# Optimization experiments

Hardware: AMD Instinct MI355X
Metric: run time of the kernel (lower is better)

The kernel has to match this reference:

```python
import jax, jax.numpy as jnp
import numpy as np

NBITS = 8          # attn_nbits
GROUP = 32         # per-group size along head_dim for Q/K quantizers
H = 16             # num_heads
EPS = 1e-8


def _ste(x, q):
    # straight-through estimator: forward=q, backward=identity
    return x + jax.lax.stop_gradient(q - x)


def pg_dynamic_quant(x, group_size=GROUP, nbits=NBITS):
    """Per-group symmetric dynamic fake-quant along last dim (ActPGDynamicQuantizer)."""
    qmax = 2.0 ** (nbits - 1) - 1
    lead, D = x.shape[:-1], x.shape[-1]
    xg = x.reshape(*lead, D // group_size, group_size)
    s = jnp.maximum(jnp.max(jnp.abs(xg), axis=-1, keepdims=True) / qmax, EPS)
    q = jnp.clip(jnp.round(xg / s), -qmax - 1.0, qmax) * s
    return _ste(x, q.reshape(x.shape))


def dynamic_quant(x, axis=2, nbits=NBITS):
    """Symmetric dynamic fake-quant, scale shared along `axis` (ActDynamicQuantizer)."""
    qmax = 2.0 ** (nbits - 1) - 1
    s = jnp.maximum(jnp.max(jnp.abs(x), axis=axis, keepdims=True) / qmax, EPS)
    q = jnp.clip(jnp.round(x / s), -qmax - 1.0, qmax) * s
    return _ste(x, q)


def static_scale_quant(x, nbits=NBITS):
    """Unsigned static-scale fake-quant for softmax map in [0,1] (ActStaticScaleQuantizer)."""
    qmax = 2.0 ** nbits - 1
    q = jnp.clip(jnp.round(x * qmax), 0.0, qmax) / qmax
    return _ste(x, q)


def setup_inputs() -> dict:
    key = jax.random.key(0)
    ks = jax.random.split(key, 7)
    B, L, C = 4, 1024, 1024
    return {
        "x":         jax.random.normal(ks[0], (B, L, C), jnp.float32),
        "attn_bias": jax.random.normal(ks[1], (1, 1, L, L), jnp.float32) * 0.1,
        "w_qkv":     jax.random.normal(ks[2], (3 * C, C), jnp.float32) * 0.02,
        "q_bias":    jax.random.normal(ks[3], (C,), jnp.float32) * 0.02,
        "v_bias":    jax.random.normal(ks[4], (C,), jnp.float32) * 0.02,
        "w_proj":    jax.random.normal(ks[5], (C, C), jnp.float32) * 0.02,
        "b_proj":    jax.random.normal(ks[6], (C,), jnp.float32) * 0.02,
    }


def reference(x, attn_bias, w_qkv, q_bias, v_bias, w_proj, b_proj):
    B, L, C = x.shape
    D = C // H
    scale = D ** -0.5
    # qkv projection: bias-free linear + concat(q_bias, zeros_k, v_bias)
    bias = jnp.concatenate([q_bias, jnp.zeros_like(q_bias), v_bias])
    qkv = (x @ w_qkv.T + bias).reshape(B, L, 3, H, D)
    q, k, v = jnp.transpose(qkv, (2, 0, 3, 1, 4))  # each [B,H,L,D]
    # inline fake-quantization (MODE 0 inference path)
    qq = pg_dynamic_quant(q)
    kk = pg_dynamic_quant(k)
    vv = dynamic_quant(v, axis=2)
    attn = jnp.einsum('bhld,bhmd->bhlm', qq * scale, kk) + attn_bias  # [B,H,L,L]
    a = jax.nn.softmax(attn, axis=-1)
    a = static_scale_quant(a)
    out = jnp.einsum('bhlm,bhmd->bhld', a, vv)
    out = jnp.transpose(out, (0, 2, 1, 3)).reshape(B, L, C)
    return out @ w_proj.T + b_proj
```

## Files before the change

### kernel.cpp

```cpp
#include <hip/hip_runtime.h>


typedef unsigned short u16;
typedef unsigned int u32;
typedef __attribute__((ext_vector_type(8))) _Float16 half8;
typedef __attribute__((ext_vector_type(4))) float f32x4;

__device__ __forceinline__ u16 f2b(float f) {
    u32 i;
    __builtin_memcpy(&i, &f, 4);
    return (u16)((i + 0x7FFFu + ((i >> 16) & 1u)) >> 16);
}

__device__ __forceinline__ void split16(float v, u16& hi, u16& lo) {
    _Float16 h = (_Float16)v;
    _Float16 l = (_Float16)(v - (float)h);
    __builtin_memcpy(&hi, &h, 2);
    __builtin_memcpy(&lo, &l, 2);
}

__device__ __forceinline__ int dot4(int a, int b, int c) {
#if __has_builtin(__builtin_amdgcn_sdot4)
    return __builtin_amdgcn_sdot4(a, b, c, false);
#else
    int r = c;
    r += ((a << 24) >> 24) * ((b << 24) >> 24);
    r += ((a << 16) >> 24) * ((b << 16) >> 24);
    r += ((a << 8) >> 24) * ((b << 8) >> 24);
    r += (a >> 24) * (b >> 24);
    return r;
#endif
}

__device__ __forceinline__ double fexp(double x) {
    double kd = rint(x * 1.4426950408889634);
    double r = fma(kd, -6.93147180369123816490e-01, x);
    r = fma(kd, -1.90821492927058770002e-10, r);
    double p = 2.7557319223985888e-07;
    p = fma(p, r, 2.7557319223985890e-06);
    p = fma(p, r, 2.4801587301587302e-05);
    p = fma(p, r, 1.9841269841269841e-04);
    p = fma(p, r, 1.3888888888888889e-03);
    p = fma(p, r, 8.3333333333333333e-03);
    p = fma(p, r, 4.1666666666666664e-02);
    p = fma(p, r, 1.6666666666666666e-01);
    p = fma(p, r, 0.5);
    p = fma(p, r, 1.0);
    p = fma(p, r, 1.0);
    long long bits;
    __builtin_memcpy(&bits, &p, 8);
    bits += ((long long)kd) << 52;
    double e;
    __builtin_memcpy(&e, &bits, 8);
    return (x < -700.0) ? 0.0 : e;
}

__global__ __launch_bounds__(256) void cvt_bf16w(u16* __restrict__ dst,
                                                 const float* __restrict__ src, int n) {
    int i = (blockIdx.x * 256 + threadIdx.x) * 4;
    if (i + 3 < n) {
        float4 v = *(const float4*)(src + i);
        ushort4 o;
        o.x = f2b(v.x); o.y = f2b(v.y); o.z = f2b(v.z); o.w = f2b(v.w);
        *(ushort4*)(dst + i) = o;
    }
}

__global__ __launch_bounds__(256) void gemm_qkv3(const float* __restrict__ A,
                                                 const float* __restrict__ Bm,
                                                 const float* __restrict__ qbias,
                                                 const float* __restrict__ vbias,
                                                 float* __restrict__ qws,
                                                 float* __restrict__ kws,
                                                 float* __restrict__ vws) {
    __shared__ u16 Ah[128 * 32], Al[128 * 32], Bh[64 * 32], Bl[64 * 32];
    const int t = threadIdx.x;
    const int lane = t & 63, w = t >> 6;
    const int srow = t >> 2, scol = (t & 3) * 8;
    const int lm = lane & 15, lk = (lane >> 4) * 8;
    const int bm = blockIdx.y, bn = blockIdx.x;

    const float* ap = A + (size_t)(bm * 128 + srow) * 1024 + scol;
    const float* bp = Bm + (size_t)(bn * 64 + srow) * 1024 + scol;

    double dacc[2][4][4];
#pragma unroll
    for (int i = 0; i < 2; i++)
#pragma unroll
        for (int j = 0; j < 4; j++)
#pragma unroll
            for (int r = 0; r < 4; r++) dacc[i][j][r] = 0.0;

    for (int slab = 0; slab < 8; slab++) {
        f32x4 acc[2][4];
#pragma unroll
        for (int i = 0; i < 2; i++)
#pragma unroll
            for (int j = 0; j < 4; j++) acc[i][j] = (f32x4){0.f, 0.f, 0.f, 0.f};

        for (int kc = 0; kc < 4; kc++) {
            const int k0 = slab * 128 + kc * 32;
            float vreg[3][8];
#pragma unroll
            for (int e = 0; e < 3; e++) {
                const float* src = (e < 2) ? (ap + e * (size_t)64 * 1024 + k0)
                                           : (bp + k0);
                float4 v0 = *(const float4*)(src);
                float4 v1 = *(const float4*)(src + 4);
                vreg[e][0] = v0.x; vreg[e][1] = v0.y; vreg[e][2] = v0.z; vreg[e][3] = v0.w;
                vreg[e][4] = v1.x; vreg[e][5] = v1.y; vreg[e][6] = v1.z; vreg[e][7] = v1.w;
            }
            __syncthreads();
#pragma unroll
            for (int e = 0; e < 3; e++) {
                union { u16 us[8]; uint4 v; } ph, pl;
#pragma unroll
                for (int j = 0; j < 8; j++) split16(vreg[e][j], ph.us[j], pl.us[j]);
                u16* dh = (e < 2) ? Ah : Bh;
                u16* dl = (e < 2) ? Al : Bl;
                int row = (e < 2) ? (srow + e * 64) : srow;
                *(uint4*)(dh + row * 32 + scol) = ph.v;
                *(uint4*)(dl + row * 32 + scol) = pl.v;
            }
            __syncthreads();

            half8 fah[2], fal[2], fbh[4], fbl[4];
#pragma unroll
            for (int i = 0; i < 2; i++) {
                int ra = (w * 32 + i * 16 + lm) * 32 + lk;
                fah[i] = *(const half8*)(Ah + ra);
                fal[i] = *(const half8*)(Al + ra);
            }
#pragma unroll
            for (int i = 0; i < 4; i++) {
                int rb = (i * 16 + lm) * 32 + lk;
                fbh[i] = *(const half8*)(Bh + rb);
                fbl[i] = *(const half8*)(Bl + rb);
            }
#pragma unroll
            for (int mi = 0; mi < 2; mi++)
#pragma unroll
                for (int ni = 0; ni < 4; ni++) {
                    acc[mi][ni] = __builtin_amdgcn_mfma_f32_16x16x32_f16(
                        fal[mi], fbh[ni], acc[mi][ni], 0, 0, 0);
                    acc[mi][ni] = __builtin_amdgcn_mfma_f32_16x16x32_f16(
                        fah[mi], fbl[ni], acc[mi][ni], 0, 0, 0);
                    acc[mi][ni] = __builtin_amdgcn_mfma_f32_16x16x32_f16(
                        fah[mi], fbh[ni], acc[mi][ni], 0, 0, 0);
                }
        }
#pragma unroll
        for (int i = 0; i < 2; i++)
#pragma unroll
            for (int j = 0; j < 4; j++)
#pragma unroll
                for (int r = 0; r < 4; r++) dacc[i][j][r] += (double)acc[i][j][r];
    }

    const int rbase = bm * 128 + w * 32 + (lane >> 4) * 4;
    const int cbase = bn * 64 + lm;
#pragma unroll
    for (int mi = 0; mi < 2; mi++)
#pragma unroll
        for (int ni = 0; ni < 4; ni++) {
            int col = cbase + ni * 16;
            int sel = col >> 10, cc = col & 1023;
            double bias = (sel == 0) ? (double)qbias[cc]
                        : ((sel == 2) ? (double)vbias[cc] : 0.0);
            float* dst = (sel == 0) ? qws : ((sel == 1) ? kws : vws);
#pragma unroll
            for (int r = 0; r < 4; r++) {
                int row = rbase + mi * 16 + r;
                dst[(size_t)row * 1024 + cc] = (float)(dacc[mi][ni][r] + bias);
            }
        }
}

__global__ __launch_bounds__(256) void quant_qk(const float* __restrict__ pre,
                                                signed char* __restrict__ qout,
                                                double* __restrict__ sout) {
    size_t g = (size_t)blockIdx.x * 256 + threadIdx.x;
    const float* p = pre + g * 32;
    float v[32];
    float amax = 0.f;
#pragma unroll
    for (int i = 0; i < 8; i++) {
        float4 q4 = ((const float4*)p)[i];
        v[i * 4 + 0] = q4.x; v[i * 4 + 1] = q4.y; v[i * 4 + 2] = q4.z; v[i * 4 + 3] = q4.w;
        amax = fmaxf(amax, fmaxf(fmaxf(fabsf(q4.x), fabsf(q4.y)),
                                 fmaxf(fabsf(q4.z), fabsf(q4.w))));
    }
    double s = fmax((double)amax / 127.0, 1e-8);
    sout[g] = s;
    int pk[8];
#pragma unroll
    for (int i = 0; i < 8; i++) {
        int b0 = (int)fmin(fmax(rint((double)v[i * 4 + 0] / s), -128.0), 127.0);
        int b1 = (int)fmin(fmax(rint((double)v[i * 4 + 1] / s), -128.0), 127.0);
        int b2 = (int)fmin(fmax(rint((double)v[i * 4 + 2] / s), -128.0), 127.0);
        int b3 = (int)fmin(fmax(rint((double)v[i * 4 + 3] / s), -128.0), 127.0);
        pk[i] = (b0 & 255) | ((b1 & 255) << 8) | ((b2 & 255) << 16) | ((b3 & 255) << 24);
    }
    int4* d = (int4*)(qout + g * 32);
    d[0] = make_int4(pk[0], pk[1], pk[2], pk[3]);
    d[1] = make_int4(pk[4], pk[5], pk[6], pk[7]);
}

__global__ __launch_bounds__(256) void quant_k(const float* __restrict__ pre,
                                               int* __restrict__ kT,
                                               double* __restrict__ ksT) {
    size_t g = (size_t)blockIdx.x * 256 + threadIdx.x;
    const float* p = pre + g * 32;
    float v[32];
    float amax = 0.f;
#pragma unroll
    for (int i = 0; i < 8; i++) {
        float4 q4 = ((const float4*)p)[i];
        v[i * 4 + 0] = q4.x; v[i * 4 + 1] = q4.y; v[i * 4 + 2] = q4.z; v[i * 4 + 3] = q4.w;
        amax = fmaxf(amax, fmaxf(fmaxf(fabsf(q4.x), fabsf(q4.y)),
                                 fmaxf(fabsf(q4.z), fabsf(q4.w))));
    }
    double s = fmax((double)amax / 127.0, 1e-8);
    int pk[8];
#pragma unroll
    for (int i = 0; i < 8; i++) {
        int b0 = (int)fmin(fmax(rint((double)v[i * 4 + 0] / s), -128.0), 127.0);
        int b1 = (int)fmin(fmax(rint((double)v[i * 4 + 1] / s), -128.0), 127.0);
        int b2 = (int)fmin(fmax(rint((double)v[i * 4 + 2] / s), -128.0), 127.0);
        int b3 = (int)fmin(fmax(rint((double)v[i * 4 + 3] / s), -128.0), 127.0);
        pk[i] = (b0 & 255) | ((b1 & 255) << 8) | ((b2 & 255) << 16) | ((b3 & 255) << 24);
    }
    const int m = (int)((g >> 5) & 1023);
    const int b = (int)(g >> 15);
    const int sub = (int)(g & 31);
    const int h = sub >> 1, pp = sub & 1;
    const int bh = b * 16 + h;
    int* dst = kT + ((size_t)bh * 16 + pp * 8) * 1024 + m;
#pragma unroll
    for (int i = 0; i < 8; i++) dst[i * 1024] = pk[i];
    ksT[((size_t)bh * 2 + pp) * 1024 + m] = s;
}

__global__ __launch_bounds__(256) void vmax_part(const float* __restrict__ vws,
                                                 float* __restrict__ pmax) {
    const int lc = blockIdx.x, b = blockIdx.y, t = threadIdx.x;
#pragma unroll
    for (int j = 0; j < 4; j++) {
        int cc = t + j * 256;
        float mx = 0.f;
        for (int l = 0; l < 16; l++)
            mx = fmaxf(mx, fabsf(vws[((size_t)(b * 1024 + lc * 16 + l)) * 1024 + cc]));
        pmax[(size_t)(b * 64 + lc) * 1024 + cc] = mx;
    }
}

__global__ __launch_bounds__(256) void vmax_final(const float* __restrict__ pmax,
                                                  double* __restrict__ vs) {
    int id = blockIdx.x * 256 + threadIdx.x;
    int b = id >> 10, cc = id & 1023;
    float mx = 0.f;
    for (int p = 0; p < 64; p++)
        mx = fmaxf(mx, pmax[(size_t)(b * 64 + p) * 1024 + cc]);
    vs[id] = fmax((double)mx / 127.0, 1e-8);
}

__global__ __launch_bounds__(256) void vquant(float* __restrict__ vws,
                                              const double* __restrict__ vs) {
    size_t e = ((size_t)blockIdx.x * 256 + threadIdx.x) * 4;
    int b = (int)(e >> 20), cc = (int)(e & 1023);
    float4 v = *(const float4*)(vws + e);
    double s0 = vs[b * 1024 + cc], s1 = vs[b * 1024 + cc + 1];
    double s2 = vs[b * 1024 + cc + 2], s3 = vs[b * 1024 + cc + 3];
    float4 o;
    o.x = (float)(fmin(fmax(rint((double)v.x / s0), -128.0), 127.0) * s0);
    o.y = (float)(fmin(fmax(rint((double)v.y / s1), -128.0), 127.0) * s1);
    o.z = (float)(fmin(fmax(rint((double)v.z / s2), -128.0), 127.0) * s2);
    o.w = (float)(fmin(fmax(rint((double)v.w / s3), -128.0), 127.0) * s3);
    *(float4*)(vws + e) = o;
}

__global__ __launch_bounds__(256) void attn(const signed char* __restrict__ qint,
                                            const int* __restrict__ kT,
                                            const double* __restrict__ qs,
                                            const double* __restrict__ ksT,
                                            const float* __restrict__ vfq,
                                            const float* __restrict__ abias,
                                            u16* __restrict__ ctx) {
    __shared__ int    kTs[16][256];
    __shared__ double ks0s[256], ks1s[256];
    __shared__ u32    packed[4][512];
    const int t = threadIdx.x;
    const int wv = t >> 6, lane = t & 63;
    const int qt = blockIdx.x, h = blockIdx.y, b = blockIdx.z;
    const int row = qt * 4 + wv;
    const size_t qrow = (size_t)(b * 1024 + row);
    const int bh = b * 16 + h;

    const int* qv = (const int*)(qint + qrow * 1024 + h * 64);
    int qd[16];
#pragma unroll
    for (int j = 0; j < 4; j++) {
        int4 tmp = ((const int4*)qv)[j];
        qd[j * 4 + 0] = tmp.x; qd[j * 4 + 1] = tmp.y;
        qd[j * 4 + 2] = tmp.z; qd[j * 4 + 3] = tmp.w;
    }
    const double sq0 = qs[qrow * 32 + 2 * h], sq1 = qs[qrow * 32 + 2 * h + 1];
    const int* kTg = kT + (size_t)bh * 16384;
    const double* ks0g = ksT + (size_t)(bh * 2) * 1024;
    const double* ks1g = ksT + (size_t)(bh * 2 + 1) * 1024;
    const float* ab = abias + (size_t)row * 1024;

    double sd[16];
    for (int c = 0; c < 4; c++) {
        if (c) __syncthreads();
#pragma unroll
        for (int r = 0; r < 4; r++) {
            const int j = wv * 4 + r;
            int4 val = *(const int4*)(kTg + (size_t)j * 1024 + c * 256 + 4 * lane);
            *(int4*)(&kTs[j][4 * lane]) = val;
        }
        ks0s[t] = ks0g[c * 256 + t];
        ks1s[t] = ks1g[c * 256 + t];
        __syncthreads();
#pragma unroll
        for (int s = 0; s < 4; s++) {
            const int ml = s * 64 + lane;
            int I0 = 0, I1 = 0;
#pragma unroll
            for (int j = 0; j < 8; j++)  I0 = dot4(qd[j], kTs[j][ml], I0);
#pragma unroll
            for (int j = 8; j < 16; j++) I1 = dot4(qd[j], kTs[j][ml], I1);
            sd[c * 4 + s] = 0.125 * (sq0 * ks0s[ml] * (double)I0
                                   + sq1 * ks1s[ml] * (double)I1)
                          + (double)ab[c * 256 + ml];
        }
    }

    double mx = sd[0];
#pragma unroll
    for (int it = 1; it < 16; it++) mx = fmax(mx, sd[it]);
#pragma unroll
    for (int off = 1; off < 64; off <<= 1) mx = fmax(mx, __shfl_xor(mx, off));
    double sum = 0.0;
#pragma unroll
    for (int it = 0; it < 16; it++) {
        double e = fexp(sd[it] - mx);
        sd[it] = e;
        sum += e;
    }
#pragma unroll
    for (int off = 1; off < 64; off <<= 1) sum += __shfl_xor(sum, off);
    const double inv = 1.0 / sum;

    int base = 0;
#pragma unroll
    for (int it = 0; it < 16; it++) {
        double a = sd[it] * inv;
        double nd = fmin(fmax(rint(a * 255.0), 0.0), 255.0);
        int ni = (int)nd;
        unsigned long long mk = __ballot(ni != 0);
        if (ni != 0) {
            int pos = base + (int)__popcll(mk & ((1ull << lane) - 1ull));
            packed[wv][pos] = ((u32)ni << 16) | (u32)(it * 64 + lane);
        }
        base += (int)__popcll(mk);
    }
    __syncthreads();

    float acc = 0.f;
    const float* vcol = vfq + ((size_t)b * 1024) * 1024 + h * 64 + lane;
    for (int j = 0; j < base; ++j) {
        u32 p = packed[wv][j];
        float a = (float)(p >> 16) / 255.0f;
        acc = fmaf(a, vcol[(size_t)(p & 1023u) * 1024], acc);
    }
    ctx[qrow * 1024 + h * 64 + lane] = f2b(acc);
}

__global__ __launch_bounds__(256) void gemm_proj(const u16* __restrict__ ctx,
                                                 const u16* __restrict__ wproj,
                                                 const float* __restrict__ bproj,
                                                 float* __restrict__ out) {
    typedef __attribute__((ext_vector_type(8))) short short8;
    __shared__ u16 As[128 * 32], Bs[128 * 32];
    f32x4 acc[4][4];
#pragma unroll
    for (int i = 0; i < 4; i++)
#pragma unroll
        for (int j = 0; j < 4; j++) acc[i][j] = (f32x4){0.f, 0.f, 0.f, 0.f};

    const int t = threadIdx.x;
    const int lane = t & 63, w = t >> 6;
    const int wm = w >> 1, wn = w & 1;
    const int srow = t >> 2, scol = (t & 3) * 8;
    const int lm = lane & 15, lk = (lane >> 4) * 8;
    const int bm = blockIdx.y, bn = blockIdx.x;
    const u16* ap = ctx + (size_t)(bm * 128 + srow) * 1024 + scol;
    const u16* bp = wproj + (size_t)(bn * 128 + srow) * 1024 + scol;

    for (int k0 = 0; k0 < 1024; k0 += 32) {
        uint4 a0 = *(const uint4*)(ap + k0);
        uint4 a1 = *(const uint4*)(ap + (size_t)64 * 1024 + k0);
        uint4 b0 = *(const uint4*)(bp + k0);
        uint4 b1 = *(const uint4*)(bp + (size_t)64 * 1024 + k0);
        __syncthreads();
        *(uint4*)(As + srow * 32 + scol) = a0;
        *(uint4*)(As + (srow + 64) * 32 + scol) = a1;
        *(uint4*)(Bs + srow * 32 + scol) = b0;
        *(uint4*)(Bs + (srow + 64) * 32 + scol) = b1;
        __syncthreads();
        short8 af[4], bfr[4];
#pragma unroll
        for (int i = 0; i < 4; i++) {
            af[i]  = *(const short8*)(As + (wm * 64 + i * 16 + lm) * 32 + lk);
            bfr[i] = *(const short8*)(Bs + (wn * 64 + i * 16 + lm) * 32 + lk);
        }
#pragma unroll
        for (int mi = 0; mi < 4; mi++)
#pragma unroll
            for (int ni = 0; ni < 4; ni++)
                acc[mi][ni] = __builtin_amdgcn_mfma_f32_16x16x32_bf16(
                    af[mi], bfr[ni], acc[mi][ni], 0, 0, 0);
    }

    const int rbase = bm * 128 + wm * 64 + (lane >> 4) * 4;
    const int cbase = bn * 128 + wn * 64 + lm;
#pragma unroll
    for (int mi = 0; mi < 4; mi++)
#pragma unroll
        for (int ni = 0; ni < 4; ni++) {
            int col = cbase + ni * 16;
            float bias = bproj[col];
#pragma unroll
            for (int r = 0; r < 4; r++) {
                int row = rbase + mi * 16 + r;
                out[(size_t)row * 1024 + col] = acc[mi][ni][r] + bias;
            }
        }
}

extern "C" void kernel_launch(void* const* d_in, const int* in_sizes, int n_in,
                              void* d_out, int out_size, void* d_ws, size_t ws_size,
                              hipStream_t stream) {
    const float* x     = (const float*)d_in[0];
    const float* abias = (const float*)d_in[1];
    const float* wqkv  = (const float*)d_in[2];
    const float* qbias = (const float*)d_in[3];
    const float* vbias = (const float*)d_in[4];
    const float* wproj = (const float*)d_in[5];
    const float* bproj = (const float*)d_in[6];
    float* out = (float*)d_out;

    char* ws = (char*)d_ws;
    float*       qpre    = (float*)(ws + 0);
    float*       kpre    = (float*)(ws + 16777216);
    float*       vfq     = (float*)(ws + 33554432);
    u16*         wprojbf = (u16*)  (ws + 50331648);
    signed char* qint    = (signed char*)(ws + 52428800);
    int*         kT      = (int*)  (ws + 56623104);
    double*      qs      = (double*)(ws + 60817408);
    double*      ksT     = (double*)(ws + 61865984);
    double*      vs      = (double*)(ws + 62914560);
    float*       pmax    = (float*)(ws + 62947328);
    u16*         ctx     = (u16*)(ws + 0);

    cvt_bf16w<<<1024, 256, 0, stream>>>(wprojbf, wproj, 1048576);
    gemm_qkv3<<<dim3(48, 32), 256, 0, stream>>>(x, wqkv, qbias, vbias,
                                                qpre, kpre, vfq);
    quant_qk<<<512, 256, 0, stream>>>(qpre, qint, qs);
    quant_k<<<512, 256, 0, stream>>>(kpre, kT, ksT);
    vmax_part<<<dim3(64, 4), 256, 0, stream>>>(vfq, pmax);
    vmax_final<<<16, 256, 0, stream>>>(pmax, vs);
    vquant<<<4096, 256, 0, stream>>>(vfq, vs);
    attn<<<dim3(256, 16, 4), 256, 0, stream>>>(qint, kT, qs, ksT, vfq, abias, ctx);
    gemm_proj<<<dim3(8, 32), 256, 0, stream>>>(ctx, wprojbf, bproj, out);
}
```

Baseline: 524.6 us.

## Split attention into score and int8 MFMA AV kernels with quantized V

The fused attention kernel used a sparse scalar gather over fp32 V. It is replaced by two kernels per batch. The first writes the 8-bit softmax probabilities, offset by 128, to a scratch buffer. The second computes P·V with int8 MFMA against a transposed int8 V, then adds back the offset through precomputed V column sums and rescales in double. This turns the memory-bound gather into a dense integer matrix product, at the cost of extra global traffic for P, per-byte scattered writes in vquant, and serialized launches per batch.

After: 803.2 us. +53.1%, slower.

```diff
diff --git a/kernel.cpp b/kernel.cpp
--- a/kernel.cpp
+++ b/kernel.cpp
@@ -5,6 +5,7 @@
 typedef unsigned int u32;
 typedef __attribute__((ext_vector_type(8))) _Float16 half8;
 typedef __attribute__((ext_vector_type(4))) float f32x4;
+typedef __attribute__((ext_vector_type(4))) int i32x4;
 
 __device__ __forceinline__ u16 f2b(float f) {
     u32 i;
@@ -264,34 +265,52 @@
     vs[id] = fmax((double)mx / 127.0, 1e-8);
 }
 
-__global__ __launch_bounds__(256) void vquant(float* __restrict__ vws,
-                                              const double* __restrict__ vs) {
+__global__ __launch_bounds__(256) void vquant(const float* __restrict__ vraw,
+                                              const double* __restrict__ vs,
+                                              signed char* __restrict__ ivt) {
     size_t e = ((size_t)blockIdx.x * 256 + threadIdx.x) * 4;
-    int b = (int)(e >> 20), cc = (int)(e & 1023);
-    float4 v = *(const float4*)(vws + e);
+    int b = (int)(e >> 20), cc = (int)(e & 1023), m = (int)((e >> 10) & 1023);
+    float4 v = *(const float4*)(vraw + e);
     double s0 = vs[b * 1024 + cc], s1 = vs[b * 1024 + cc + 1];
     double s2 = vs[b * 1024 + cc + 2], s3 = vs[b * 1024 + cc + 3];
-    float4 o;
-    o.x = (float)(fmin(fmax(rint((double)v.x / s0), -128.0), 127.0) * s0);
-    o.y = (float)(fmin(fmax(rint((double)v.y / s1), -128.0), 127.0) * s1);
-    o.z = (float)(fmin(fmax(rint((double)v.z / s2), -128.0), 127.0) * s2);
-    o.w = (float)(fmin(fmax(rint((double)v.w / s3), -128.0), 127.0) * s3);
-    *(float4*)(vws + e) = o;
-}
-
-__global__ __launch_bounds__(256) void attn(const signed char* __restrict__ qint,
-                                            const int* __restrict__ kT,
-                                            const double* __restrict__ qs,
-                                            const double* __restrict__ ksT,
-                                            const float* __restrict__ vfq,
-                                            const float* __restrict__ abias,
-                                            u16* __restrict__ ctx) {
+    int i0 = (int)fmin(fmax(rint((double)v.x / s0), -128.0), 127.0);
+    int i1 = (int)fmin(fmax(rint((double)v.y / s1), -128.0), 127.0);
+    int i2 = (int)fmin(fmax(rint((double)v.z / s2), -128.0), 127.0);
+    int i3 = (int)fmin(fmax(rint((double)v.w / s3), -128.0), 127.0);
+    size_t base = ((size_t)b * 1024 + cc) * 1024 + m;
+    ivt[base]          = (signed char)i0;
+    ivt[base + 1024]   = (signed char)i1;
+    ivt[base + 2048]   = (signed char)i2;
+    ivt[base + 3072]   = (signed char)i3;
+}
+
+__global__ __launch_bounds__(256) void colsum_k(const signed char* __restrict__ ivt,
+                                                int* __restrict__ csum) {
+    int id = blockIdx.x * 256 + threadIdx.x;
+    const int4* p = (const int4*)(ivt + (size_t)id * 1024);
+    int s = 0;
+    for (int i = 0; i < 64; i++) {
+        int4 w = p[i];
+        s = dot4(w.x, 0x01010101, s);
+        s = dot4(w.y, 0x01010101, s);
+        s = dot4(w.z, 0x01010101, s);
+        s = dot4(w.w, 0x01010101, s);
+    }
+    csum[id] = s;
+}
+
+__global__ __launch_bounds__(256) void attn_sc(const signed char* __restrict__ qint,
+                                               const int* __restrict__ kT,
+                                               const double* __restrict__ qs,
+                                               const double* __restrict__ ksT,
+                                               const float* __restrict__ abias,
+                                               signed char* __restrict__ Pp,
+                                               int b) {
     __shared__ int    kTs[16][256];
     __shared__ double ks0s[256], ks1s[256];
-    __shared__ u32    packed[4][512];
     const int t = threadIdx.x;
     const int wv = t >> 6, lane = t & 63;
-    const int qt = blockIdx.x, h = blockIdx.y, b = blockIdx.z;
+    const int qt = blockIdx.x, h = blockIdx.y;
     const int row = qt * 4 + wv;
     const size_t qrow = (size_t)(b * 1024 + row);
     const int bh = b * 16 + h;
@@ -352,29 +371,66 @@
     for (int off = 1; off < 64; off <<= 1) sum += __shfl_xor(sum, off);
     const double inv = 1.0 / sum;
 
-    int base = 0;
+    signed char* prow = Pp + ((size_t)h * 1024 + row) * 1024;
 #pragma unroll
     for (int it = 0; it < 16; it++) {
         double a = sd[it] * inv;
         double nd = fmin(fmax(rint(a * 255.0), 0.0), 255.0);
         int ni = (int)nd;
-        unsigned long long mk = __ballot(ni != 0);
-        if (ni != 0) {
-            int pos = base + (int)__popcll(mk & ((1ull << lane) - 1ull));
-            packed[wv][pos] = ((u32)ni << 16) | (u32)(it * 64 + lane);
-        }
-        base += (int)__popcll(mk);
+        prow[it * 64 + lane] = (signed char)(ni - 128);
+    }
+}
+
+__global__ __launch_bounds__(256) void attn_av(const signed char* __restrict__ Pp,
+                                               const signed char* __restrict__ ivt,
+                                               const double* __restrict__ vs,
+                                               const int* __restrict__ csum,
+                                               u16* __restrict__ ctx,
+                                               int b) {
+    __shared__ __align__(16) signed char Pl[16 * 1024];
+    const int t = threadIdx.x;
+    const int wv = t >> 6, lane = t & 63;
+    const int qt = blockIdx.x, h = blockIdx.y;
+
+    {
+        const int row = t >> 4, seg = t & 15;
+        const signed char* src = Pp + ((size_t)h * 1024 + qt * 16 + row) * 1024 + seg * 64;
+        const int x = (row & 7) << 3;
+#pragma unroll
+        for (int g = 0; g < 4; g++) {
+            long lo = *(const long*)(src + g * 16);
+            long hi = *(const long*)(src + g * 16 + 8);
+            int m0 = seg * 64 + g * 16;
+            *(long*)(&Pl[row * 1024 + (m0 ^ x)]) = lo;
+            *(long*)(&Pl[row * 1024 + ((m0 + 8) ^ x)]) = hi;
+        }
     }
     __syncthreads();
 
-    float acc = 0.f;
-    const float* vcol = vfq + ((size_t)b * 1024) * 1024 + h * 64 + lane;
-    for (int j = 0; j < base; ++j) {
-        u32 p = packed[wv][j];
-        float a = (float)(p >> 16) / 255.0f;
-        acc = fmaf(a, vcol[(size_t)(p & 1023u) * 1024], acc);
-    }
-    ctx[qrow * 1024 + h * 64 + lane] = f2b(acc);
+    const int col = lane & 15;
+    const int cc = h * 64 + wv * 16 + col;
+    const signed char* brow = ivt + ((size_t)b * 1024 + cc) * 1024;
+    const int arow = lane & 15;
+    const int xr = (arow & 7) << 3;
+    const int kq = (lane >> 4) * 8;
+
+    i32x4 acc = (i32x4){0, 0, 0, 0};
+#pragma unroll
+    for (int k0 = 0; k0 < 1024; k0 += 32) {
+        long a = *(const long*)(&Pl[arow * 1024 + ((k0 + kq) ^ xr)]);
+        long bv = *(const long*)(brow + k0 + kq);
+        acc = __builtin_amdgcn_mfma_i32_16x16x32_i8(a, bv, acc, 0, 0, 0);
+    }
+
+    const double sc = vs[b * 1024 + cc] * (1.0 / 255.0);
+    const int cs = 128 * csum[b * 1024 + cc];
+    const int rbase = qt * 16 + (lane >> 4) * 4;
+#pragma unroll
+    for (int r = 0; r < 4; r++) {
+        int S = acc[r] + cs;
+        double val = (double)S * sc;
+        ctx[((size_t)(b * 1024) + rbase + r) * 1024 + cc] = f2b((float)val);
+    }
 }
 
 __global__ __launch_bounds__(256) void gemm_proj(const u16* __restrict__ ctx,
@@ -454,7 +510,7 @@
     char* ws = (char*)d_ws;
     float*       qpre    = (float*)(ws + 0);
     float*       kpre    = (float*)(ws + 16777216);
-    float*       vfq     = (float*)(ws + 33554432);
+    float*       vraw    = (float*)(ws + 33554432);
     u16*         wprojbf = (u16*)  (ws + 50331648);
     signed char* qint    = (signed char*)(ws + 52428800);
     int*         kT      = (int*)  (ws + 56623104);
@@ -463,15 +519,22 @@
     double*      vs      = (double*)(ws + 62914560);
     float*       pmax    = (float*)(ws + 62947328);
     u16*         ctx     = (u16*)(ws + 0);
+    signed char* ivt     = (signed char*)(ws + 16777216);
+    signed char* Pp      = (signed char*)(ws + 33554432);
+    int*         csum    = (int*)(ws + 62947328);
 
     cvt_bf16w<<<1024, 256, 0, stream>>>(wprojbf, wproj, 1048576);
     gemm_qkv3<<<dim3(48, 32), 256, 0, stream>>>(x, wqkv, qbias, vbias,
-                                                qpre, kpre, vfq);
+                                                qpre, kpre, vraw);
     quant_qk<<<512, 256, 0, stream>>>(qpre, qint, qs);
     quant_k<<<512, 256, 0, stream>>>(kpre, kT, ksT);
-    vmax_part<<<dim3(64, 4), 256, 0, stream>>>(vfq, pmax);
+    vmax_part<<<dim3(64, 4), 256, 0, stream>>>(vraw, pmax);
     vmax_final<<<16, 256, 0, stream>>>(pmax, vs);
-    vquant<<<4096, 256, 0, stream>>>(vfq, vs);
-    attn<<<dim3(256, 16, 4), 256, 0, stream>>>(qint, kT, qs, ksT, vfq, abias, ctx);
+    vquant<<<4096, 256, 0, stream>>>(vraw, vs, ivt);
+    colsum_k<<<16, 256, 0, stream>>>(ivt, csum);
+    for (int b = 0; b < 4; b++) {
+        attn_sc<<<dim3(256, 16), 256, 0, stream>>>(qint, kT, qs, ksT, abias, Pp, b);
+        attn_av<<<dim3(64, 16), 256, 0, stream>>>(Pp, ivt, vs, csum, ctx, b);
+    }
     gemm_proj<<<dim3(8, 32), 256, 0, stream>>>(ctx, wprojbf, bproj, out);
 }
```
